# Kernel optimization log

Measured on AMD Instinct MI355X. Metric: run time of the kernel, lower is better.

Reference implementation:

```python
import jax, jax.numpy as jnp
import numpy as np

N_NODES = 50000
N_EDGES = 800000
F_IN = 256
HIDDEN = 64
HEADS = 4
N_CLASS = 40
NEG_SLOPE = 0.2


def gat_layer(x, src, dst, W, al, ar, b, heads, out_dim):
    # x: [N, Fin] -> h: [N, H, D]
    N = x.shape[0]
    h = (x @ W).reshape(N, heads, out_dim)
    el = jnp.sum(h * al, axis=-1)  # [N, H]
    er = jnp.sum(h * ar, axis=-1)  # [N, H]
    e = jax.nn.leaky_relu(el[src] + er[dst], NEG_SLOPE)  # [E, H]
    # segment softmax over incoming edges of each destination node
    emax = jax.ops.segment_max(e, dst, num_segments=N)  # [N, H] (-inf for empty, unused)
    ex = jnp.exp(e - emax[dst])
    esum = jax.ops.segment_sum(ex, dst, num_segments=N)
    alpha = ex / esum[dst]  # [E, H]; esum[dst] >= ex > 0 per existing edge
    msg = h[src] * alpha[:, :, None]  # [E, H, D]
    out = jax.ops.segment_sum(msg, dst, num_segments=N)  # [N, H, D]
    return out + b.reshape(1, heads, out_dim)


def setup_inputs() -> dict:
    key = jax.random.key(0)
    ks = jax.random.split(key, 16)
    x = jax.random.normal(ks[0], (N_NODES, F_IN), dtype=jnp.float32)
    edge_index = jax.random.randint(ks[1], (2, N_EDGES), 0, N_NODES, dtype=jnp.int64)
    s = 0.1
    return {
        "x": x,
        "edge_index": edge_index,
        "W1": jax.random.normal(ks[2], (F_IN, HEADS * HIDDEN), dtype=jnp.float32) * s,
        "al1": jax.random.normal(ks[3], (HEADS, HIDDEN), dtype=jnp.float32) * s,
        "ar1": jax.random.normal(ks[4], (HEADS, HIDDEN), dtype=jnp.float32) * s,
        "b1": jnp.zeros((HEADS * HIDDEN,), dtype=jnp.float32),
        "W2": jax.random.normal(ks[5], (HEADS * HIDDEN, HEADS * HIDDEN), dtype=jnp.float32) * s,
        "al2": jax.random.normal(ks[6], (HEADS, HIDDEN), dtype=jnp.float32) * s,
        "ar2": jax.random.normal(ks[7], (HEADS, HIDDEN), dtype=jnp.float32) * s,
        "b2": jnp.zeros((HEADS * HIDDEN,), dtype=jnp.float32),
        "W3": jax.random.normal(ks[8], (HEADS * HIDDEN, N_CLASS), dtype=jnp.float32) * s,
        "al3": jax.random.normal(ks[9], (1, N_CLASS), dtype=jnp.float32) * s,
        "ar3": jax.random.normal(ks[10], (1, N_CLASS), dtype=jnp.float32) * s,
        "b3": jnp.zeros((N_CLASS,), dtype=jnp.float32),
    }


def reference(x, edge_index, W1, al1, ar1, b1, W2, al2, ar2, b2, W3, al3, ar3, b3):
    src, dst = edge_index[0], edge_index[1]
    N = x.shape[0]
    # layer 1: GATConv -> flatten heads -> ELU
    h = gat_layer(x, src, dst, W1, al1, ar1, b1, HEADS, HIDDEN).reshape(N, -1)
    h = jax.nn.elu(h)
    # layer 2
    h = gat_layer(h, src, dst, W2, al2, ar2, b2, HEADS, HIDDEN).reshape(N, -1)
    h = jax.nn.elu(h)
    # layer 3: 1 head -> mean over head dim
    h = gat_layer(h, src, dst, W3, al3, ar3, b3, 1, N_CLASS).mean(axis=1)
    return jax.nn.log_softmax(h, axis=1)
```

## Files before the change

kernel.cpp:

```cpp
#include <hip/hip_runtime.h>
#include <hip/hip_bf16.h>
#include <math.h>

#define N_NODES 50000
#define N_EDGES 800000
#define NCLASS 40

using f32x4 = __attribute__((ext_vector_type(4))) float;
using s16x8 = __attribute__((ext_vector_type(8))) short;

__global__ void detect_i64(const int* __restrict__ raw, int* __restrict__ flag) {
  int t = threadIdx.x;
  int v = raw[2 * t + 1];
  unsigned long long any = __ballot(v != 0);
  if (t == 0) flag[0] = (any == 0ULL) ? 1 : 0;
}

__global__ void norm_count(const int* __restrict__ raw, const int* __restrict__ flag,
                           int* __restrict__ s32, int* __restrict__ d32,
                           int* __restrict__ deg) {
  int e = blockIdx.x * blockDim.x + threadIdx.x;
  if (e >= N_EDGES) return;
  int s, d;
  if (flag[0]) {
    s = raw[2 * e];
    d = raw[2 * N_EDGES + 2 * e];
  } else {
    s = raw[e];
    d = raw[N_EDGES + e];
  }
  s32[e] = s;
  d32[e] = d;
  atomicAdd(&deg[d], 1);
}

__global__ void scan_bsum(const int* __restrict__ deg, int* __restrict__ bsums) {
  __shared__ int sm[256];
  int t = threadIdx.x;
  int i = blockIdx.x * 256 + t;
  sm[t] = (i < N_NODES) ? deg[i] : 0;
  __syncthreads();
  for (int off = 128; off > 0; off >>= 1) {
    if (t < off) sm[t] += sm[t + off];
    __syncthreads();
  }
  if (t == 0) bsums[blockIdx.x] = sm[0];
}

__global__ void scan_offsets(int* __restrict__ bsums, int* __restrict__ rowp, int nb) {
  __shared__ int sm[256];
  int t = threadIdx.x;
  int v = (t < nb) ? bsums[t] : 0;
  sm[t] = v;
  __syncthreads();
  for (int off = 1; off < 256; off <<= 1) {
    int add = (t >= off) ? sm[t - off] : 0;
    __syncthreads();
    sm[t] += add;
    __syncthreads();
  }
  if (t < nb) bsums[t] = sm[t] - v;
  if (t == 0) rowp[N_NODES] = N_EDGES;
}

__global__ void scan_final(const int* __restrict__ deg, const int* __restrict__ bsums,
                           int* __restrict__ rowp, int* __restrict__ cursor) {
  __shared__ int sm[256];
  int t = threadIdx.x;
  int i = blockIdx.x * 256 + t;
  int v = (i < N_NODES) ? deg[i] : 0;
  sm[t] = v;
  __syncthreads();
  for (int off = 1; off < 256; off <<= 1) {
    int add = (t >= off) ? sm[t - off] : 0;
    __syncthreads();
    sm[t] += add;
    __syncthreads();
  }
  int excl = sm[t] - v + bsums[blockIdx.x];
  if (i < N_NODES) { rowp[i] = excl; cursor[i] = excl; }
}

__global__ void scatter_edges(const int* __restrict__ s32, const int* __restrict__ d32,
                              int* __restrict__ cursor, int* __restrict__ srcs) {
  int e = blockIdx.x * blockDim.x + threadIdx.x;
  if (e >= N_EDGES) return;
  int d = d32[e];
  int pos = atomicAdd(&cursor[d], 1);
  srcs[pos] = s32[e];
}

__global__ void tr_w(const float* __restrict__ W, __hip_bfloat16* __restrict__ WT) {
  int id = blockIdx.x * 256 + threadIdx.x;
  int n = id >> 8, k = id & 255;
  WT[n * 256 + k] = __float2bfloat16(W[k * 256 + n]);
}

__global__ void tr_w3(const float* __restrict__ W3, __hip_bfloat16* __restrict__ WT3) {
  int id = blockIdx.x * 256 + threadIdx.x;
  int n = id >> 8, k = id & 255;
  WT3[n * 256 + k] = (n < NCLASS) ? __float2bfloat16(W3[k * NCLASS + n]) : __float2bfloat16(0.f);
}

__global__ void cast_x(const float* __restrict__ x, __hip_bfloat16* __restrict__ xb) {
  int id = blockIdx.x * 256 + threadIdx.x;
  float4 v = *reinterpret_cast<const float4*>(x + (size_t)id * 4);
  ushort4 u;
  __hip_bfloat16 b;
  b = __float2bfloat16(v.x); u.x = *(unsigned short*)&b;
  b = __float2bfloat16(v.y); u.y = *(unsigned short*)&b;
  b = __float2bfloat16(v.z); u.z = *(unsigned short*)&b;
  b = __float2bfloat16(v.w); u.w = *(unsigned short*)&b;
  *reinterpret_cast<ushort4*>((unsigned short*)xb + (size_t)id * 4) = u;
}

__global__ __launch_bounds__(256) void gemm_gat12(const __hip_bfloat16* __restrict__ A,
                                                  const __hip_bfloat16* __restrict__ WT,
                                                  const float* __restrict__ al,
                                                  const float* __restrict__ ar,
                                                  __hip_bfloat16* __restrict__ hb,
                                                  float* __restrict__ el,
                                                  float* __restrict__ er) {
  constexpr int MREP = 4, NREP = 4;
  __shared__ __align__(16) __hip_bfloat16 As[128][40];
  __shared__ __align__(16) __hip_bfloat16 Bs[128][40];

  int t = threadIdx.x;
  int lane = t & 63, wave = t >> 6;
  int wr = wave >> 1, wc = wave & 1;
  int row0 = blockIdx.x * 128, col0 = blockIdx.y * 128;
  int ln = lane & 15;
  int kc8 = (lane >> 4) * 8;

  f32x4 acc[MREP][NREP];
  const f32x4 fz = {0.f, 0.f, 0.f, 0.f};
#pragma unroll
  for (int m = 0; m < MREP; ++m)
#pragma unroll
    for (int n = 0; n < NREP; ++n) acc[m][n] = fz;

  for (int k0 = 0; k0 < 256; k0 += 32) {
#pragma unroll
    for (int it = 0; it < 2; ++it) {
      int c = t + it * 256;
      int r = c >> 2, kc = (c & 3) * 8;
      int grow = row0 + r;
      f32x4 v = fz;
      if (grow < N_NODES)
        v = *reinterpret_cast<const f32x4*>(A + (size_t)grow * 256 + k0 + kc);
      *reinterpret_cast<f32x4*>(&As[r][kc]) = v;
    }
#pragma unroll
    for (int it = 0; it < 2; ++it) {
      int c = t + it * 256;
      int r = c >> 2, kc = (c & 3) * 8;
      f32x4 v = *reinterpret_cast<const f32x4*>(WT + (size_t)(col0 + r) * 256 + k0 + kc);
      *reinterpret_cast<f32x4*>(&Bs[r][kc]) = v;
    }
    __syncthreads();
    s16x8 af[MREP], bfr[NREP];
#pragma unroll
    for (int m = 0; m < MREP; ++m)
      af[m] = *reinterpret_cast<const s16x8*>(&As[wr * 64 + m * 16 + ln][kc8]);
#pragma unroll
    for (int n = 0; n < NREP; ++n)
      bfr[n] = *reinterpret_cast<const s16x8*>(&Bs[wc * 64 + n * 16 + ln][kc8]);
#pragma unroll
    for (int m = 0; m < MREP; ++m)
#pragma unroll
      for (int n = 0; n < NREP; ++n)
        acc[m][n] = __builtin_amdgcn_mfma_f32_16x16x32_bf16(af[m], bfr[n], acc[m][n], 0, 0, 0);
    __syncthreads();
  }

  int head = blockIdx.y * 2 + wc;
  float alv[NREP], arv[NREP];
#pragma unroll
  for (int n = 0; n < NREP; ++n) {
    int c = head * 64 + n * 16 + ln;
    alv[n] = al[c];
    arv[n] = ar[c];
  }
#pragma unroll
  for (int m = 0; m < MREP; ++m) {
#pragma unroll
    for (int r = 0; r < 4; ++r) {
      int row = row0 + wr * 64 + m * 16 + (lane >> 4) * 4 + r;
      bool ok = row < N_NODES;
      float pl = 0.f, pr = 0.f;
#pragma unroll
      for (int n = 0; n < NREP; ++n) {
        float v = acc[m][n][r];
        pl += v * alv[n];
        pr += v * arv[n];
        if (ok) hb[(size_t)row * 256 + head * 64 + n * 16 + ln] = __float2bfloat16(v);
      }
      for (int off = 1; off < 16; off <<= 1) {
        pl += __shfl_xor(pl, off);
        pr += __shfl_xor(pr, off);
      }
      if (ln == 0 && ok) {
        el[row * 4 + head] = pl;
        er[row * 4 + head] = pr;
      }
    }
  }
}

__global__ __launch_bounds__(256) void gemm_gat3(const __hip_bfloat16* __restrict__ A,
                                                 const __hip_bfloat16* __restrict__ WT,
                                                 const float* __restrict__ al,
                                                 const float* __restrict__ ar,
                                                 float* __restrict__ h3,
                                                 float* __restrict__ el,
                                                 float* __restrict__ er) {
  constexpr int MREP = 2, NREP = 4;
  __shared__ __align__(16) __hip_bfloat16 As[128][40];
  __shared__ __align__(16) __hip_bfloat16 Bs[64][40];

  int t = threadIdx.x;
  int lane = t & 63, wave = t >> 6;
  int row0 = blockIdx.x * 128;
  int ln = lane & 15;
  int kc8 = (lane >> 4) * 8;

  f32x4 acc[MREP][NREP];
  const f32x4 fz = {0.f, 0.f, 0.f, 0.f};
#pragma unroll
  for (int m = 0; m < MREP; ++m)
#pragma unroll
    for (int n = 0; n < NREP; ++n) acc[m][n] = fz;

  for (int k0 = 0; k0 < 256; k0 += 32) {
#pragma unroll
    for (int it = 0; it < 2; ++it) {
      int c = t + it * 256;
      int r = c >> 2, kc = (c & 3) * 8;
      int grow = row0 + r;
      f32x4 v = fz;
      if (grow < N_NODES)
        v = *reinterpret_cast<const f32x4*>(A + (size_t)grow * 256 + k0 + kc);
      *reinterpret_cast<f32x4*>(&As[r][kc]) = v;
    }
    {
      int c = t;
      int r = c >> 2, kc = (c & 3) * 8;
      f32x4 v = *reinterpret_cast<const f32x4*>(WT + (size_t)r * 256 + k0 + kc);
      *reinterpret_cast<f32x4*>(&Bs[r][kc]) = v;
    }
    __syncthreads();
    s16x8 af[MREP], bfr[NREP];
#pragma unroll
    for (int m = 0; m < MREP; ++m)
      af[m] = *reinterpret_cast<const s16x8*>(&As[wave * 32 + m * 16 + ln][kc8]);
#pragma unroll
    for (int n = 0; n < NREP; ++n)
      bfr[n] = *reinterpret_cast<const s16x8*>(&Bs[n * 16 + ln][kc8]);
#pragma unroll
    for (int m = 0; m < MREP; ++m)
#pragma unroll
      for (int n = 0; n < NREP; ++n)
        acc[m][n] = __builtin_amdgcn_mfma_f32_16x16x32_bf16(af[m], bfr[n], acc[m][n], 0, 0, 0);
    __syncthreads();
  }

  float alv[NREP], arv[NREP];
#pragma unroll
  for (int n = 0; n < NREP; ++n) {
    int c = n * 16 + ln;
    alv[n] = (c < NCLASS) ? al[c] : 0.f;
    arv[n] = (c < NCLASS) ? ar[c] : 0.f;
  }
#pragma unroll
  for (int m = 0; m < MREP; ++m) {
#pragma unroll
    for (int r = 0; r < 4; ++r) {
      int row = row0 + wave * 32 + m * 16 + (lane >> 4) * 4 + r;
      bool ok = row < N_NODES;
      float pl = 0.f, pr = 0.f;
#pragma unroll
      for (int n = 0; n < NREP; ++n) {
        float v = acc[m][n][r];
        pl += v * alv[n];
        pr += v * arv[n];
        if (ok) h3[(size_t)row * 64 + n * 16 + ln] = v;
      }
      for (int off = 1; off < 16; off <<= 1) {
        pl += __shfl_xor(pl, off);
        pr += __shfl_xor(pr, off);
      }
      if (ln == 0 && ok) {
        el[row] = pl;
        er[row] = pr;
      }
    }
  }
}

__global__ __launch_bounds__(64) void alpha_heads(const float* __restrict__ el,
                                                  const float* __restrict__ er,
                                                  const int* __restrict__ rowp,
                                                  const int* __restrict__ srcs,
                                                  float* __restrict__ alpha) {
  int n = blockIdx.x;
  int lane = threadIdx.x;
  int head = lane & 3, slot = lane >> 2;
  int i0 = rowp[n], i1 = rowp[n + 1];
  float ern = er[n * 4 + head];
  float m = -1e30f, l = 0.f;
  for (int base = i0; base < i1; base += 16) {
    int i = base + slot;
    float e = -1e30f;
    if (i < i1) {
      int s = srcs[i];
      e = el[s * 4 + head] + ern;
      e = (e >= 0.f) ? e : 0.2f * e;
      alpha[(size_t)i * 4 + head] = e;
    }
    float nm = fmaxf(m, e);
    l = l * __expf(m - nm) + ((i < i1) ? __expf(e - nm) : 0.f);
    m = nm;
  }
  for (int off = 4; off <= 32; off <<= 1) {
    float mo = __shfl_xor(m, off);
    float lo = __shfl_xor(l, off);
    float nm = fmaxf(m, mo);
    l = l * __expf(m - nm) + lo * __expf(mo - nm);
    m = nm;
  }
  float inv = (l > 0.f) ? (1.f / l) : 0.f;
  for (int base = i0; base < i1; base += 16) {
    int i = base + slot;
    if (i < i1) {
      float e = alpha[(size_t)i * 4 + head];
      alpha[(size_t)i * 4 + head] = __expf(e - m) * inv;
    }
  }
}

__global__ __launch_bounds__(64) void alpha_cls(const float* __restrict__ el,
                                                const float* __restrict__ er,
                                                const int* __restrict__ rowp,
                                                const int* __restrict__ srcs,
                                                float* __restrict__ alpha) {
  int n = blockIdx.x;
  int slot = threadIdx.x;
  int i0 = rowp[n], i1 = rowp[n + 1];
  float ern = er[n];
  float m = -1e30f, l = 0.f;
  for (int base = i0; base < i1; base += 64) {
    int i = base + slot;
    float e = -1e30f;
    if (i < i1) {
      int s = srcs[i];
      e = el[s] + ern;
      e = (e >= 0.f) ? e : 0.2f * e;
      alpha[i] = e;
    }
    float nm = fmaxf(m, e);
    l = l * __expf(m - nm) + ((i < i1) ? __expf(e - nm) : 0.f);
    m = nm;
  }
  for (int off = 1; off <= 32; off <<= 1) {
    float mo = __shfl_xor(m, off);
    float lo = __shfl_xor(l, off);
    float nm = fmaxf(m, mo);
    l = l * __expf(m - nm) + lo * __expf(mo - nm);
    m = nm;
  }
  float inv = (l > 0.f) ? (1.f / l) : 0.f;
  for (int base = i0; base < i1; base += 64) {
    int i = base + slot;
    if (i < i1) alpha[i] = __expf(alpha[i] - m) * inv;
  }
}

__global__ __launch_bounds__(128) void agg_gather(const __hip_bfloat16* __restrict__ hb,
                                                  const float* __restrict__ alpha,
                                                  const float* __restrict__ bias,
                                                  const int* __restrict__ rowp,
                                                  const int* __restrict__ srcs,
                                                  __hip_bfloat16* __restrict__ ob) {
  int n = blockIdx.x, t = threadIdx.x;
  int head = t >> 5;
  const unsigned int* hp = (const unsigned int*)hb;
  int i0 = rowp[n], i1 = rowp[n + 1];
  float ax0 = 0.f, ax1 = 0.f, ax2 = 0.f, ax3 = 0.f;
  float ay0 = 0.f, ay1 = 0.f, ay2 = 0.f, ay3 = 0.f;
  int i = i0;
  for (; i + 3 < i1; i += 4) {
    int s0 = srcs[i], s1 = srcs[i + 1], s2 = srcs[i + 2], s3 = srcs[i + 3];
    float a0 = alpha[(size_t)i * 4 + head];
    float a1 = alpha[(size_t)(i + 1) * 4 + head];
    float a2 = alpha[(size_t)(i + 2) * 4 + head];
    float a3 = alpha[(size_t)(i + 3) * 4 + head];
    unsigned int w0 = hp[(size_t)s0 * 128 + t];
    unsigned int w1 = hp[(size_t)s1 * 128 + t];
    unsigned int w2 = hp[(size_t)s2 * 128 + t];
    unsigned int w3 = hp[(size_t)s3 * 128 + t];
    ax0 += a0 * __uint_as_float(w0 << 16);
    ay0 += a0 * __uint_as_float(w0 & 0xffff0000u);
    ax1 += a1 * __uint_as_float(w1 << 16);
    ay1 += a1 * __uint_as_float(w1 & 0xffff0000u);
    ax2 += a2 * __uint_as_float(w2 << 16);
    ay2 += a2 * __uint_as_float(w2 & 0xffff0000u);
    ax3 += a3 * __uint_as_float(w3 << 16);
    ay3 += a3 * __uint_as_float(w3 & 0xffff0000u);
  }
  for (; i < i1; ++i) {
    int s0 = srcs[i];
    float a0 = alpha[(size_t)i * 4 + head];
    unsigned int w0 = hp[(size_t)s0 * 128 + t];
    ax0 += a0 * __uint_as_float(w0 << 16);
    ay0 += a0 * __uint_as_float(w0 & 0xffff0000u);
  }
  float v0 = ax0 + ax1 + ax2 + ax3 + bias[2 * t];
  float v1 = ay0 + ay1 + ay2 + ay3 + bias[2 * t + 1];
  v0 = (v0 > 0.f) ? v0 : (__expf(v0) - 1.f);
  v1 = (v1 > 0.f) ? v1 : (__expf(v1) - 1.f);
  __hip_bfloat16 b0 = __float2bfloat16(v0), b1 = __float2bfloat16(v1);
  unsigned int packed = (unsigned int)(*(unsigned short*)&b0) |
                        ((unsigned int)(*(unsigned short*)&b1) << 16);
  ((unsigned int*)ob)[(size_t)n * 128 + t] = packed;
}

__global__ __launch_bounds__(64) void agg_cls(const float* __restrict__ h3,
                                              const float* __restrict__ alpha,
                                              const float* __restrict__ bias,
                                              const int* __restrict__ rowp,
                                              const int* __restrict__ srcs,
                                              float* __restrict__ out) {
  int n = blockIdx.x, t = threadIdx.x;
  bool act = t < NCLASS;
  int i0 = rowp[n], i1 = rowp[n + 1];
  float acc0 = 0.f, acc1 = 0.f;
  int i = i0;
  for (; i + 1 < i1; i += 2) {
    int s0 = srcs[i], s1 = srcs[i + 1];
    float a0 = alpha[i], a1 = alpha[i + 1];
    if (act) {
      acc0 += a0 * h3[(size_t)s0 * 64 + t];
      acc1 += a1 * h3[(size_t)s1 * 64 + t];
    }
  }
  if (i < i1 && act) acc0 += alpha[i] * h3[(size_t)srcs[i] * 64 + t];
  float z = acc0 + acc1 + (act ? bias[t] : 0.f);
  float zz = act ? z : -INFINITY;
  float mx = zz;
  for (int off = 32; off > 0; off >>= 1) mx = fmaxf(mx, __shfl_xor(mx, off));
  float ex = act ? __expf(z - mx) : 0.f;
  float sum = ex;
  for (int off = 32; off > 0; off >>= 1) sum += __shfl_xor(sum, off);
  if (act) out[(size_t)n * NCLASS + t] = z - mx - __logf(sum);
}

extern "C" void kernel_launch(void* const* d_in, const int* in_sizes, int n_in,
                              void* d_out, int out_size, void* d_ws, size_t ws_size,
                              hipStream_t stream) {
  const float* x   = (const float*)d_in[0];
  const int* edges = (const int*)d_in[1];
  const float* W1  = (const float*)d_in[2];
  const float* al1 = (const float*)d_in[3];
  const float* ar1 = (const float*)d_in[4];
  const float* b1  = (const float*)d_in[5];
  const float* W2  = (const float*)d_in[6];
  const float* al2 = (const float*)d_in[7];
  const float* ar2 = (const float*)d_in[8];
  const float* b2  = (const float*)d_in[9];
  const float* W3  = (const float*)d_in[10];
  const float* al3 = (const float*)d_in[11];
  const float* ar3 = (const float*)d_in[12];
  const float* b3  = (const float*)d_in[13];
  float* out = (float*)d_out;

  const size_t N = N_NODES, E = N_EDGES;
  float* h3 = (float*)d_ws;
  float* el = h3 + N * 64;
  float* er = el + N * 4;
  float* alpha = er + N * 4;
  __hip_bfloat16* xb = (__hip_bfloat16*)(alpha + E * 4);
  __hip_bfloat16* hb = xb + N * 256;
  __hip_bfloat16* ob = hb + N * 256;
  __hip_bfloat16* WT = ob + N * 256;
  __hip_bfloat16* WT3 = WT + 256 * 256;
  int* rowp   = (int*)(WT3 + 64 * 256);
  int* cursor = rowp + (N + 1);
  int* srcs   = cursor + N;
  int* deg    = srcs + E;
  int* bsums  = deg + N;
  int* s32    = bsums + 256;
  int* d32    = s32 + E;
  int* flag   = d32 + E;
  float* alpha3 = (float*)s32;

  hipMemsetAsync(deg, 0, N * sizeof(int), stream);
  detect_i64<<<1, 64, 0, stream>>>(edges, flag);
  int eb = (int)((E + 255) / 256);
  norm_count<<<eb, 256, 0, stream>>>(edges, flag, s32, d32, deg);
  int nb = (int)((N + 255) / 256);
  scan_bsum<<<nb, 256, 0, stream>>>(deg, bsums);
  scan_offsets<<<1, 256, 0, stream>>>(bsums, rowp, nb);
  scan_final<<<nb, 256, 0, stream>>>(deg, bsums, rowp, cursor);
  scatter_edges<<<eb, 256, 0, stream>>>(s32, d32, cursor, srcs);

  dim3 gg((unsigned)((N + 127) / 128), 2);
  dim3 g3((unsigned)((N + 127) / 128), 1);

  cast_x<<<(unsigned)(N * 256 / 4 / 256), 256, 0, stream>>>(x, xb);
  tr_w<<<256, 256, 0, stream>>>(W1, WT);
  gemm_gat12<<<gg, 256, 0, stream>>>(xb, WT, al1, ar1, hb, el, er);
  alpha_heads<<<(unsigned)N, 64, 0, stream>>>(el, er, rowp, srcs, alpha);
  agg_gather<<<(unsigned)N, 128, 0, stream>>>(hb, alpha, b1, rowp, srcs, ob);
  tr_w<<<256, 256, 0, stream>>>(W2, WT);
  gemm_gat12<<<gg, 256, 0, stream>>>(ob, WT, al2, ar2, hb, el, er);
  alpha_heads<<<(unsigned)N, 64, 0, stream>>>(el, er, rowp, srcs, alpha);
  agg_gather<<<(unsigned)N, 128, 0, stream>>>(hb, alpha, b2, rowp, srcs, ob);
  tr_w3<<<64, 256, 0, stream>>>(W3, WT3);
  gemm_gat3<<<g3, 256, 0, stream>>>(ob, WT3, al3, ar3, h3, el, er);
  alpha_cls<<<(unsigned)N, 64, 0, stream>>>(el, er, rowp, srcs, alpha3);
  agg_cls<<<(unsigned)N, 64, 0, stream>>>(h3, alpha3, b3, rowp, srcs, out);
}
```

Measured before the change: 500.1 us.

## Fuse segment softmax into gather aggregation and store layer-3 features as bf16

Merges the per-node attention softmax kernels into the aggregation kernels. Edge scores are computed, max/sum-reduced and normalised in shared memory (up to 512 edges per node, recomputed from el beyond that), so the alpha array in global memory is no longer written and read back, and three launches go away. Layer-3 features are also stored as bf16 instead of fp32, halving the gather traffic in the final aggregation. Each block now does the softmax reduction itself with a couple of barriers, and layer-3 precision drops slightly.

```diff
diff --git a/kernel.cpp b/kernel.cpp
--- a/kernel.cpp
+++ b/kernel.cpp
@@ -5,6 +5,7 @@
 #define N_NODES 50000
 #define N_EDGES 800000
 #define NCLASS 40
+#define MAXE 512
 
 using f32x4 = __attribute__((ext_vector_type(4))) float;
 using s16x8 = __attribute__((ext_vector_type(8))) short;
@@ -211,9 +212,9 @@
                                                  const __hip_bfloat16* __restrict__ WT,
                                                  const float* __restrict__ al,
                                                  const float* __restrict__ ar,
-                                                 float* __restrict__ h3,
-                                                 float* __restrict__ el,
-                                                 float* __restrict__ er) {
+                                                 __hip_bfloat16* __restrict__ h3b,
+                                                 float* __restrict__ el3,
+                                                 float* __restrict__ er3) {
   constexpr int MREP = 2, NREP = 4;
   __shared__ __align__(16) __hip_bfloat16 As[128][40];
   __shared__ __align__(16) __hip_bfloat16 Bs[64][40];
@@ -283,139 +284,108 @@
         float v = acc[m][n][r];
         pl += v * alv[n];
         pr += v * arv[n];
-        if (ok) h3[(size_t)row * 64 + n * 16 + ln] = v;
+        if (ok) h3b[(size_t)row * 64 + n * 16 + ln] = __float2bfloat16(v);
       }
       for (int off = 1; off < 16; off <<= 1) {
         pl += __shfl_xor(pl, off);
         pr += __shfl_xor(pr, off);
       }
       if (ln == 0 && ok) {
-        el[row] = pl;
-        er[row] = pr;
+        el3[row] = pl;
+        er3[row] = pr;
       }
     }
   }
 }
 
-__global__ __launch_bounds__(64) void alpha_heads(const float* __restrict__ el,
-                                                  const float* __restrict__ er,
-                                                  const int* __restrict__ rowp,
-                                                  const int* __restrict__ srcs,
-                                                  float* __restrict__ alpha) {
-  int n = blockIdx.x;
-  int lane = threadIdx.x;
-  int head = lane & 3, slot = lane >> 2;
-  int i0 = rowp[n], i1 = rowp[n + 1];
+__global__ __launch_bounds__(128) void agg_fused(const __hip_bfloat16* __restrict__ hb,
+                                                 const float* __restrict__ el,
+                                                 const float* __restrict__ er,
+                                                 const float* __restrict__ bias,
+                                                 const int* __restrict__ rowp,
+                                                 const int* __restrict__ srcs,
+                                                 __hip_bfloat16* __restrict__ ob) {
+  __shared__ float eld[MAXE * 5];
+  __shared__ float mi[8];
+  int n = blockIdx.x, t = threadIdx.x;
+  int head = t >> 5, slot = t & 31;
+  int i0 = rowp[n], deg = rowp[n + 1] - i0;
   float ern = er[n * 4 + head];
   float m = -1e30f, l = 0.f;
-  for (int base = i0; base < i1; base += 16) {
-    int i = base + slot;
-    float e = -1e30f;
-    if (i < i1) {
-      int s = srcs[i];
-      e = el[s * 4 + head] + ern;
-      e = (e >= 0.f) ? e : 0.2f * e;
-      alpha[(size_t)i * 4 + head] = e;
-    }
+  for (int j = slot; j < deg; j += 32) {
+    int s = srcs[i0 + j];
+    float e = el[s * 4 + head] + ern;
+    e = (e >= 0.f) ? e : 0.2f * e;
+    if (j < MAXE) eld[j * 5 + head] = e;
     float nm = fmaxf(m, e);
-    l = l * __expf(m - nm) + ((i < i1) ? __expf(e - nm) : 0.f);
+    l = l * __expf(m - nm) + __expf(e - nm);
     m = nm;
   }
-  for (int off = 4; off <= 32; off <<= 1) {
-    float mo = __shfl_xor(m, off);
-    float lo = __shfl_xor(l, off);
+  for (int off = 1; off < 32; off <<= 1) {
+    float mo = __shfl_xor(m, off), lo = __shfl_xor(l, off);
     float nm = fmaxf(m, mo);
     l = l * __expf(m - nm) + lo * __expf(mo - nm);
     m = nm;
   }
   float inv = (l > 0.f) ? (1.f / l) : 0.f;
-  for (int base = i0; base < i1; base += 16) {
-    int i = base + slot;
-    if (i < i1) {
-      float e = alpha[(size_t)i * 4 + head];
-      alpha[(size_t)i * 4 + head] = __expf(e - m) * inv;
-    }
-  }
-}
-
-__global__ __launch_bounds__(64) void alpha_cls(const float* __restrict__ el,
-                                                const float* __restrict__ er,
-                                                const int* __restrict__ rowp,
-                                                const int* __restrict__ srcs,
-                                                float* __restrict__ alpha) {
-  int n = blockIdx.x;
-  int slot = threadIdx.x;
-  int i0 = rowp[n], i1 = rowp[n + 1];
-  float ern = er[n];
-  float m = -1e30f, l = 0.f;
-  for (int base = i0; base < i1; base += 64) {
-    int i = base + slot;
-    float e = -1e30f;
-    if (i < i1) {
-      int s = srcs[i];
-      e = el[s] + ern;
-      e = (e >= 0.f) ? e : 0.2f * e;
-      alpha[i] = e;
-    }
-    float nm = fmaxf(m, e);
-    l = l * __expf(m - nm) + ((i < i1) ? __expf(e - nm) : 0.f);
-    m = nm;
-  }
-  for (int off = 1; off <= 32; off <<= 1) {
-    float mo = __shfl_xor(m, off);
-    float lo = __shfl_xor(l, off);
-    float nm = fmaxf(m, mo);
-    l = l * __expf(m - nm) + lo * __expf(mo - nm);
-    m = nm;
-  }
-  float inv = (l > 0.f) ? (1.f / l) : 0.f;
-  for (int base = i0; base < i1; base += 64) {
-    int i = base + slot;
-    if (i < i1) alpha[i] = __expf(alpha[i] - m) * inv;
-  }
-}
-
-__global__ __launch_bounds__(128) void agg_gather(const __hip_bfloat16* __restrict__ hb,
-                                                  const float* __restrict__ alpha,
-                                                  const float* __restrict__ bias,
-                                                  const int* __restrict__ rowp,
-                                                  const int* __restrict__ srcs,
-                                                  __hip_bfloat16* __restrict__ ob) {
-  int n = blockIdx.x, t = threadIdx.x;
-  int head = t >> 5;
+  if (slot == 0) { mi[head] = m; mi[4 + head] = inv; }
+  __syncthreads();
+  int ecount = (deg < MAXE) ? deg : MAXE;
+  for (int k = t; k < ecount * 4; k += 128) {
+    int j = k >> 2, hh = k & 3;
+    eld[j * 5 + hh] = __expf(eld[j * 5 + hh] - mi[hh]) * mi[4 + hh];
+  }
+  __syncthreads();
   const unsigned int* hp = (const unsigned int*)hb;
-  int i0 = rowp[n], i1 = rowp[n + 1];
   float ax0 = 0.f, ax1 = 0.f, ax2 = 0.f, ax3 = 0.f;
   float ay0 = 0.f, ay1 = 0.f, ay2 = 0.f, ay3 = 0.f;
-  int i = i0;
-  for (; i + 3 < i1; i += 4) {
-    int s0 = srcs[i], s1 = srcs[i + 1], s2 = srcs[i + 2], s3 = srcs[i + 3];
-    float a0 = alpha[(size_t)i * 4 + head];
-    float a1 = alpha[(size_t)(i + 1) * 4 + head];
-    float a2 = alpha[(size_t)(i + 2) * 4 + head];
-    float a3 = alpha[(size_t)(i + 3) * 4 + head];
-    unsigned int w0 = hp[(size_t)s0 * 128 + t];
-    unsigned int w1 = hp[(size_t)s1 * 128 + t];
-    unsigned int w2 = hp[(size_t)s2 * 128 + t];
-    unsigned int w3 = hp[(size_t)s3 * 128 + t];
-    ax0 += a0 * __uint_as_float(w0 << 16);
-    ay0 += a0 * __uint_as_float(w0 & 0xffff0000u);
-    ax1 += a1 * __uint_as_float(w1 << 16);
-    ay1 += a1 * __uint_as_float(w1 & 0xffff0000u);
-    ax2 += a2 * __uint_as_float(w2 << 16);
-    ay2 += a2 * __uint_as_float(w2 & 0xffff0000u);
-    ax3 += a3 * __uint_as_float(w3 << 16);
-    ay3 += a3 * __uint_as_float(w3 & 0xffff0000u);
-  }
-  for (; i < i1; ++i) {
-    int s0 = srcs[i];
-    float a0 = alpha[(size_t)i * 4 + head];
-    unsigned int w0 = hp[(size_t)s0 * 128 + t];
-    ax0 += a0 * __uint_as_float(w0 << 16);
-    ay0 += a0 * __uint_as_float(w0 & 0xffff0000u);
-  }
-  float v0 = ax0 + ax1 + ax2 + ax3 + bias[2 * t];
-  float v1 = ay0 + ay1 + ay2 + ay3 + bias[2 * t + 1];
+  int j = 0;
+  for (; j + 3 < deg; j += 4) {
+    int s0 = srcs[i0 + j], s1 = srcs[i0 + j + 1], s2 = srcs[i0 + j + 2], s3 = srcs[i0 + j + 3];
+    float w0, w1, w2, w3;
+    if (j + 3 < MAXE) {
+      w0 = eld[(j + 0) * 5 + head];
+      w1 = eld[(j + 1) * 5 + head];
+      w2 = eld[(j + 2) * 5 + head];
+      w3 = eld[(j + 3) * 5 + head];
+    } else {
+      float e0 = el[s0 * 4 + head] + ern; e0 = (e0 >= 0.f) ? e0 : 0.2f * e0;
+      float e1 = el[s1 * 4 + head] + ern; e1 = (e1 >= 0.f) ? e1 : 0.2f * e1;
+      float e2 = el[s2 * 4 + head] + ern; e2 = (e2 >= 0.f) ? e2 : 0.2f * e2;
+      float e3 = el[s3 * 4 + head] + ern; e3 = (e3 >= 0.f) ? e3 : 0.2f * e3;
+      w0 = __expf(e0 - m) * inv;
+      w1 = __expf(e1 - m) * inv;
+      w2 = __expf(e2 - m) * inv;
+      w3 = __expf(e3 - m) * inv;
+    }
+    unsigned int h0 = hp[(size_t)s0 * 128 + t];
+    unsigned int h1 = hp[(size_t)s1 * 128 + t];
+    unsigned int h2 = hp[(size_t)s2 * 128 + t];
+    unsigned int h3v = hp[(size_t)s3 * 128 + t];
+    ax0 += w0 * __uint_as_float(h0 << 16);
+    ay0 += w0 * __uint_as_float(h0 & 0xffff0000u);
+    ax1 += w1 * __uint_as_float(h1 << 16);
+    ay1 += w1 * __uint_as_float(h1 & 0xffff0000u);
+    ax2 += w2 * __uint_as_float(h2 << 16);
+    ay2 += w2 * __uint_as_float(h2 & 0xffff0000u);
+    ax3 += w3 * __uint_as_float(h3v << 16);
+    ay3 += w3 * __uint_as_float(h3v & 0xffff0000u);
+  }
+  for (; j < deg; ++j) {
+    int s0 = srcs[i0 + j];
+    float w0;
+    if (j < MAXE) {
+      w0 = eld[j * 5 + head];
+    } else {
+      float e0 = el[s0 * 4 + head] + ern; e0 = (e0 >= 0.f) ? e0 : 0.2f * e0;
+      w0 = __expf(e0 - m) * inv;
+    }
+    unsigned int h0 = hp[(size_t)s0 * 128 + t];
+    ax0 += w0 * __uint_as_float(h0 << 16);
+    ay0 += w0 * __uint_as_float(h0 & 0xffff0000u);
+  }
+  float v0 = (ax0 + ax1) + (ax2 + ax3) + bias[2 * t];
+  float v1 = (ay0 + ay1) + (ay2 + ay3) + bias[2 * t + 1];
   v0 = (v0 > 0.f) ? v0 : (__expf(v0) - 1.f);
   v1 = (v1 > 0.f) ? v1 : (__expf(v1) - 1.f);
   __hip_bfloat16 b0 = __float2bfloat16(v0), b1 = __float2bfloat16(v1);
@@ -424,34 +394,91 @@
   ((unsigned int*)ob)[(size_t)n * 128 + t] = packed;
 }
 
-__global__ __launch_bounds__(64) void agg_cls(const float* __restrict__ h3,
-                                              const float* __restrict__ alpha,
-                                              const float* __restrict__ bias,
-                                              const int* __restrict__ rowp,
-                                              const int* __restrict__ srcs,
-                                              float* __restrict__ out) {
+__global__ __launch_bounds__(64) void agg_cls_fused(const __hip_bfloat16* __restrict__ h3b,
+                                                    const float* __restrict__ el3,
+                                                    const float* __restrict__ er3,
+                                                    const float* __restrict__ bias,
+                                                    const int* __restrict__ rowp,
+                                                    const int* __restrict__ srcs,
+                                                    float* __restrict__ out) {
+  __shared__ float eldc[MAXE];
   int n = blockIdx.x, t = threadIdx.x;
-  bool act = t < NCLASS;
-  int i0 = rowp[n], i1 = rowp[n + 1];
-  float acc0 = 0.f, acc1 = 0.f;
-  int i = i0;
-  for (; i + 1 < i1; i += 2) {
-    int s0 = srcs[i], s1 = srcs[i + 1];
-    float a0 = alpha[i], a1 = alpha[i + 1];
-    if (act) {
-      acc0 += a0 * h3[(size_t)s0 * 64 + t];
-      acc1 += a1 * h3[(size_t)s1 * 64 + t];
-    }
-  }
-  if (i < i1 && act) acc0 += alpha[i] * h3[(size_t)srcs[i] * 64 + t];
-  float z = acc0 + acc1 + (act ? bias[t] : 0.f);
-  float zz = act ? z : -INFINITY;
-  float mx = zz;
+  int i0 = rowp[n], deg = rowp[n + 1] - i0;
+  float ern = er3[n];
+  float m = -1e30f, l = 0.f;
+  for (int j = t; j < deg; j += 64) {
+    int s = srcs[i0 + j];
+    float e = el3[s] + ern;
+    e = (e >= 0.f) ? e : 0.2f * e;
+    if (j < MAXE) eldc[j] = e;
+    float nm = fmaxf(m, e);
+    l = l * __expf(m - nm) + __expf(e - nm);
+    m = nm;
+  }
+  for (int off = 1; off < 64; off <<= 1) {
+    float mo = __shfl_xor(m, off), lo = __shfl_xor(l, off);
+    float nm = fmaxf(m, mo);
+    l = l * __expf(m - nm) + lo * __expf(mo - nm);
+    m = nm;
+  }
+  float inv = (l > 0.f) ? (1.f / l) : 0.f;
+  __syncthreads();
+  int ecount = (deg < MAXE) ? deg : MAXE;
+  for (int k = t; k < ecount; k += 64) eldc[k] = __expf(eldc[k] - m) * inv;
+  __syncthreads();
+  bool act2 = t < ((NCLASS + 1) / 2);
+  const unsigned int* hp3 = (const unsigned int*)h3b;
+  float ax = 0.f, ay = 0.f, bx = 0.f, by = 0.f;
+  int j = 0;
+  for (; j + 1 < deg; j += 2) {
+    int s0 = srcs[i0 + j], s1 = srcs[i0 + j + 1];
+    float w0, w1;
+    if (j + 1 < MAXE) {
+      w0 = eldc[j];
+      w1 = eldc[j + 1];
+    } else {
+      float e0 = el3[s0] + ern; e0 = (e0 >= 0.f) ? e0 : 0.2f * e0;
+      float e1 = el3[s1] + ern; e1 = (e1 >= 0.f) ? e1 : 0.2f * e1;
+      w0 = __expf(e0 - m) * inv;
+      w1 = __expf(e1 - m) * inv;
+    }
+    if (act2) {
+      unsigned int h0 = hp3[(size_t)s0 * 32 + t];
+      unsigned int h1 = hp3[(size_t)s1 * 32 + t];
+      ax += w0 * __uint_as_float(h0 << 16);
+      ay += w0 * __uint_as_float(h0 & 0xffff0000u);
+      bx += w1 * __uint_as_float(h1 << 16);
+      by += w1 * __uint_as_float(h1 & 0xffff0000u);
+    }
+  }
+  if (j < deg) {
+    int s0 = srcs[i0 + j];
+    float w0;
+    if (j < MAXE) {
+      w0 = eldc[j];
+    } else {
+      float e0 = el3[s0] + ern; e0 = (e0 >= 0.f) ? e0 : 0.2f * e0;
+      w0 = __expf(e0 - m) * inv;
+    }
+    if (act2) {
+      unsigned int h0 = hp3[(size_t)s0 * 32 + t];
+      ax += w0 * __uint_as_float(h0 << 16);
+      ay += w0 * __uint_as_float(h0 & 0xffff0000u);
+    }
+  }
+  float z0 = ax + bx + (act2 ? bias[2 * t] : 0.f);
+  float z1 = ay + by + (act2 ? bias[2 * t + 1] : 0.f);
+  float mx = act2 ? fmaxf(z0, z1) : -1e30f;
   for (int off = 32; off > 0; off >>= 1) mx = fmaxf(mx, __shfl_xor(mx, off));
-  float ex = act ? __expf(z - mx) : 0.f;
-  float sum = ex;
-  for (int off = 32; off > 0; off >>= 1) sum += __shfl_xor(sum, off);
-  if (act) out[(size_t)n * NCLASS + t] = z - mx - __logf(sum);
+  float sm = act2 ? (__expf(z0 - mx) + __expf(z1 - mx)) : 0.f;
+  for (int off = 32; off > 0; off >>= 1) sm += __shfl_xor(sm, off);
+  float ls = __logf(sm);
+  if (act2) {
+    float2 r;
+    r.x = z0 - mx - ls;
+    r.y = z1 - mx - ls;
+    *reinterpret_cast<float2*>(out + (size_t)n * NCLASS + 2 * t) = r;
+  }
 }
 
 extern "C" void kernel_launch(void* const* d_in, const int* in_sizes, int n_in,
@@ -474,14 +501,15 @@
   float* out = (float*)d_out;
 
   const size_t N = N_NODES, E = N_EDGES;
-  float* h3 = (float*)d_ws;
-  float* el = h3 + N * 64;
-  float* er = el + N * 4;
-  float* alpha = er + N * 4;
-  __hip_bfloat16* xb = (__hip_bfloat16*)(alpha + E * 4);
+  float* el  = (float*)d_ws;
+  float* er  = el + N * 4;
+  float* el3 = er + N * 4;
+  float* er3 = el3 + N;
+  __hip_bfloat16* xb = (__hip_bfloat16*)(er3 + N);
   __hip_bfloat16* hb = xb + N * 256;
   __hip_bfloat16* ob = hb + N * 256;
-  __hip_bfloat16* WT = ob + N * 256;
+  __hip_bfloat16* h3b = ob + N * 256;
+  __hip_bfloat16* WT = h3b + N * 64;
   __hip_bfloat16* WT3 = WT + 256 * 256;
   int* rowp   = (int*)(WT3 + 64 * 256);
   int* cursor = rowp + (N + 1);
@@ -491,7 +519,6 @@
   int* s32    = bsums + 256;
   int* d32    = s32 + E;
   int* flag   = d32 + E;
-  float* alpha3 = (float*)s32;
 
   hipMemsetAsync(deg, 0, N * sizeof(int), stream);
   detect_i64<<<1, 64, 0, stream>>>(edges, flag);
@@ -509,14 +536,11 @@
   cast_x<<<(unsigned)(N * 256 / 4 / 256), 256, 0, stream>>>(x, xb);
   tr_w<<<256, 256, 0, stream>>>(W1, WT);
   gemm_gat12<<<gg, 256, 0, stream>>>(xb, WT, al1, ar1, hb, el, er);
-  alpha_heads<<<(unsigned)N, 64, 0, stream>>>(el, er, rowp, srcs, alpha);
-  agg_gather<<<(unsigned)N, 128, 0, stream>>>(hb, alpha, b1, rowp, srcs, ob);
+  agg_fused<<<(unsigned)N, 128, 0, stream>>>(hb, el, er, b1, rowp, srcs, ob);
   tr_w<<<256, 256, 0, stream>>>(W2, WT);
   gemm_gat12<<<gg, 256, 0, stream>>>(ob, WT, al2, ar2, hb, el, er);
-  alpha_heads<<<(unsigned)N, 64, 0, stream>>>(el, er, rowp, srcs, alpha);
-  agg_gather<<<(unsigned)N, 128, 0, stream>>>(hb, alpha, b2, rowp, srcs, ob);
+  agg_fused<<<(unsigned)N, 128, 0, stream>>>(hb, el, er, b2, rowp, srcs, ob);
   tr_w3<<<64, 256, 0, stream>>>(W3, WT3);
-  gemm_gat3<<<g3, 256, 0, stream>>>(ob, WT3, al3, ar3, h3, el, er);
-  alpha_cls<<<(unsigned)N, 64, 0, stream>>>(el, er, rowp, srcs, alpha3);
-  agg_cls<<<(unsigned)N, 64, 0, stream>>>(h3, alpha3, b3, rowp, srcs, out);
-}
+  gemm_gat3<<<g3, 256, 0, stream>>>(ob, WT3, al3, ar3, h3b, el3, er3);
+  agg_cls_fused<<<(unsigned)N, 64, 0, stream>>>(h3b, el3, er3, b3, rowp, srcs, out);
+}
```

Result: faster. 474.3 us (-5.1%).
